# Performance work log

Hardware: AMD Instinct MI355X
Metric: run time of the kernel (lower is better)

Reference implementation:

```python
import jax, jax.numpy as jnp
import numpy as np

B, IC, H, W = 32, 128, 112, 112
OC, K, STRIDE, PAD = 256, 3, 2, 1


def setup_inputs() -> dict:
    key = jax.random.key(0)
    kx, kw = jax.random.split(key)
    x = jax.random.normal(kx, (B, IC, H, W), dtype=jnp.float32)
    weight = jax.random.normal(kw, (OC, IC, K, K), dtype=jnp.float32) * 0.01
    bias = jnp.zeros((OC,), dtype=jnp.float32)
    return {"x": x, "weight": weight, "bias": bias}


def reference(x, weight, bias):
    # Equivalent of the nested-loop conv: standard cross-correlation,
    # stride=2, zero padding=1, NCHW / OIHW layouts.
    out = jax.lax.conv_general_dilated(
        x, weight,
        window_strides=(STRIDE, STRIDE),
        padding=[(PAD, PAD), (PAD, PAD)],
        dimension_numbers=("NCHW", "OIHW", "NCHW"),
    )
    return out + bias[None, :, None, None]
```

## Files before the change

kernel.cpp:

```cpp
#include <hip/hip_runtime.h>
#include <hip/hip_bf16.h>


#define B_    32
#define IC_   128
#define H_    112
#define W_    112
#define HW_   (H_ * W_)
#define OC_   256
#define OH_   56
#define OW_   56
#define HP    113
#define NPIX  (B_ * OH_ * OW_)
#define XT_BYTES ((size_t)B_ * HP * HP * IC_ * 2)
#define WT_BYTES ((size_t)9 * OC_ * IC_ * 2)

typedef __attribute__((ext_vector_type(8))) short bf16x8;
typedef __attribute__((ext_vector_type(4))) float f32x4;

static __device__ __forceinline__ unsigned f2bf_u(float f) {
  union { float f; unsigned u; } v; v.f = f;
  return (v.u + 0x7FFF + ((v.u >> 16) & 1)) >> 16;
}

__global__ __launch_bounds__(256) void xtrans_kernel(
    const float* __restrict__ x, unsigned short* __restrict__ xt) {
  __shared__ unsigned short lds[128 * 128];
  const int ihp = blockIdx.x;
  const int b   = blockIdx.y;
  const int tid = threadIdx.x;

  if (ihp > 0) {
    const float* xp = x + (size_t)b * IC_ * HW_ + (size_t)(ihp - 1) * W_;
#pragma unroll
    for (int it = 0; it < 16; ++it) {
      const int i  = tid + it * 256;
      const int ic = i >> 5;
      const int g  = i & 31;
      if (g < 28) {
        const float4 v = *reinterpret_cast<const float4*>(
            xp + (size_t)ic * HW_ + g * 4);
        uint2 p;
        p.x = f2bf_u(v.x) | (f2bf_u(v.y) << 16);
        p.y = f2bf_u(v.z) | (f2bf_u(v.w) << 16);
        const int gs = g ^ (((ic >> 3) & 7) << 2);
        *reinterpret_cast<uint2*>(&lds[ic * 128 + gs * 4]) = p;
      }
    }
  }
  __syncthreads();

  unsigned short* xrow = xt + ((size_t)(b * HP + ihp)) * (HP * IC_);
  const bool live = (ihp > 0);
#pragma unroll
  for (int it = 0; it < 8; ++it) {
    const int e = tid + it * 256;
    if (e >= HP * 16) break;
    const int iwp = e >> 4;
    const int icg = e & 15;
    uint4 v = {0u, 0u, 0u, 0u};
    if (live && iwp > 0) {
      const int iw  = iwp - 1;
      const int col = ((iw >> 2) ^ ((icg & 7) << 2)) * 4 + (iw & 3);
      const int r0  = icg * 8;
      unsigned u0 = lds[(r0 + 0) * 128 + col];
      unsigned u1 = lds[(r0 + 1) * 128 + col];
      unsigned u2 = lds[(r0 + 2) * 128 + col];
      unsigned u3 = lds[(r0 + 3) * 128 + col];
      unsigned u4 = lds[(r0 + 4) * 128 + col];
      unsigned u5 = lds[(r0 + 5) * 128 + col];
      unsigned u6 = lds[(r0 + 6) * 128 + col];
      unsigned u7 = lds[(r0 + 7) * 128 + col];
      v.x = u0 | (u1 << 16);
      v.y = u2 | (u3 << 16);
      v.z = u4 | (u5 << 16);
      v.w = u6 | (u7 << 16);
    }
    *reinterpret_cast<uint4*>(xrow + iwp * IC_ + icg * 8) = v;
  }
}

__global__ __launch_bounds__(256) void wtrans_kernel(
    const float* __restrict__ w, unsigned short* __restrict__ wt) {
  const int t  = blockIdx.x * 256 + threadIdx.x;
  const int oc = t >> 7;
  const int ic = t & 127;
  const float* ws = w + (size_t)t * 9;
#pragma unroll
  for (int tap = 0; tap < 9; ++tap)
    wt[((size_t)tap * OC_ + oc) * IC_ + ic] = (unsigned short)f2bf_u(ws[tap]);
}

__global__ __launch_bounds__(256) void conv_mfma_kernel(
    const unsigned short* __restrict__ xt, const unsigned short* __restrict__ wt,
    const float* __restrict__ bias, float* __restrict__ out) {
  __shared__ short Ws[2][128 * 32];
  __shared__ short Xs[2][128 * 32];

  const int tid  = threadIdx.x;
  const int wav  = tid >> 6;
  const int lane = tid & 63;

  const int bid  = blockIdx.x;
  const int wgid = (bid & 7) * 196 + (bid >> 3);
  const int mt  = wgid & 1;
  const int pt  = wgid >> 1;
  const int oc0 = mt * 128;
  const int p0  = pt * 128;

  const int l2 = lane >> 2;
  const int lc = lane & 3;
  const char* xsrc[2];
  const char* wsrc[2];
#pragma unroll
  for (int i = 0; i < 2; ++i) {
    const int pix = p0 + wav * 32 + i * 16 + l2;
    const int b   = pix / 3136;
    const int q   = pix - b * 3136;
    const int oh  = q / 56;
    const int ow  = q - oh * 56;
    const size_t e = (((size_t)b * HP + 2 * oh) * HP + 2 * ow) * IC_;
    xsrc[i] = reinterpret_cast<const char*>(xt) + e * 2 + lc * 16;
    const int ocr = oc0 + wav * 32 + i * 16 + l2;
    wsrc[i] = reinterpret_cast<const char*>(wt) + (size_t)ocr * IC_ * 2 + lc * 16;
  }
  char* xdst = reinterpret_cast<char*>(&Xs[0][0]) + wav * 2048;
  char* wdst = reinterpret_cast<char*>(&Ws[0][0]) + wav * 2048;

  const int wm  = wav >> 1;
  const int wn  = wav & 1;
  const int l15 = lane & 15;
  const int kg  = (lane >> 4) * 8;
  const short* wrow = &Ws[0][0] + ((wm * 64 + l15) * 32 + kg);
  const short* xrow = &Xs[0][0] + ((wn * 64 + l15) * 32 + kg);

  f32x4 acc[4][4] = {};

  auto stage = [&](int buf, int tap, int icc) {
    const int kh = tap / 3;
    const int kw = tap - kh * 3;
    const size_t xoff = ((size_t)(kh * HP + kw) * IC_ + icc * 32) * 2;
    const size_t woff = ((size_t)tap * OC_ * IC_ + icc * 32) * 2;
    char* xd = xdst + buf * (128 * 32 * 2);
    char* wd = wdst + buf * (128 * 32 * 2);
#pragma unroll
    for (int i = 0; i < 2; ++i) {
      __builtin_amdgcn_global_load_lds(
          (const __attribute__((address_space(1))) void*)(xsrc[i] + xoff),
          (__attribute__((address_space(3))) void*)(xd + i * 1024), 16, 0, 0);
      __builtin_amdgcn_global_load_lds(
          (const __attribute__((address_space(1))) void*)(wsrc[i] + woff),
          (__attribute__((address_space(3))) void*)(wd + i * 1024), 16, 0, 0);
    }
  };

  auto compute = [&](int buf) {
    const short* wr = wrow + buf * (128 * 32);
    const short* xr = xrow + buf * (128 * 32);
    bf16x8 af[4], bfr[4];
#pragma unroll
    for (int mi = 0; mi < 4; ++mi)
      af[mi] = *reinterpret_cast<const bf16x8*>(wr + mi * 16 * 32);
#pragma unroll
    for (int ni = 0; ni < 4; ++ni)
      bfr[ni] = *reinterpret_cast<const bf16x8*>(xr + ni * 16 * 32);
#pragma unroll
    for (int mi = 0; mi < 4; ++mi)
#pragma unroll
      for (int ni = 0; ni < 4; ++ni)
        acc[mi][ni] = __builtin_amdgcn_mfma_f32_16x16x32_bf16(
            af[mi], bfr[ni], acc[mi][ni], 0, 0, 0);
  };

  stage(0, 0, 0);
  __syncthreads();

  for (int tap = 0; tap < 9; ++tap) {
    const bool lt = (tap == 8);
    stage(1, tap, 1);  compute(0);  __syncthreads();
    stage(0, tap, 2);  compute(1);  __syncthreads();
    stage(1, tap, 3);  compute(0);  __syncthreads();
    if (!lt) { stage(0, tap + 1, 0); }
    compute(1);
    if (!lt) { __syncthreads(); }
  }

#pragma unroll
  for (int mi = 0; mi < 4; ++mi) {
#pragma unroll
    for (int j = 0; j < 4; ++j) {
      const int oc = oc0 + wm * 64 + mi * 16 + (lane >> 4) * 4 + j;
      const float bv = bias[oc];
#pragma unroll
      for (int ni = 0; ni < 4; ++ni) {
        const int pix = p0 + wn * 64 + ni * 16 + l15;
        const int b   = pix / 3136;
        const int q   = pix - b * 3136;
        out[((size_t)b * OC_ + oc) * 3136 + q] = acc[mi][ni][j] + bv;
      }
    }
  }
}

__global__ __launch_bounds__(256) void conv2d_f32_kernel(
    const float* __restrict__ x, const float* __restrict__ w,
    const float* __restrict__ bias, float* __restrict__ out) {
  __shared__ float wlds[IC_ * 9][8];
  const int b   = blockIdx.z;
  const int oc0 = blockIdx.y * 8;
  const float* wsrc = w + (size_t)oc0 * (IC_ * 9);
  for (int i = threadIdx.x; i < IC_ * 9 * 8; i += 256) {
    const int j = i / (IC_ * 9);
    const int t = i - j * (IC_ * 9);
    wlds[t][j] = wsrc[(size_t)j * (IC_ * 9) + t];
  }
  __syncthreads();
  const int p  = blockIdx.x * 256 + threadIdx.x;
  const int ow = p % OW_;
  const int oh = p / OW_;
  const bool pv = (oh < OH_);
  const int ih0 = 2 * oh - 1;
  const int iw0 = 2 * ow - 1;
  const float* xb = x + (size_t)b * IC_ * HW_ + (ptrdiff_t)ih0 * W_ + iw0;
  float acc[8];
#pragma unroll
  for (int j = 0; j < 8; ++j) acc[j] = 0.f;
  for (int ic = 0; ic < IC_; ++ic) {
    const float* xc = xb + (size_t)ic * HW_;
#pragma unroll
    for (int kh = 0; kh < 3; ++kh) {
      const bool hv = pv && ((ih0 + kh) >= 0);
#pragma unroll
      for (int kw = 0; kw < 3; ++kw) {
        const bool v = hv && ((iw0 + kw) >= 0);
        const float xv = v ? xc[kh * W_ + kw] : 0.f;
        const int t = ic * 9 + kh * 3 + kw;
        const float4 w0 = *reinterpret_cast<const float4*>(&wlds[t][0]);
        const float4 w1 = *reinterpret_cast<const float4*>(&wlds[t][4]);
        acc[0] = fmaf(xv, w0.x, acc[0]); acc[1] = fmaf(xv, w0.y, acc[1]);
        acc[2] = fmaf(xv, w0.z, acc[2]); acc[3] = fmaf(xv, w0.w, acc[3]);
        acc[4] = fmaf(xv, w1.x, acc[4]); acc[5] = fmaf(xv, w1.y, acc[5]);
        acc[6] = fmaf(xv, w1.z, acc[6]); acc[7] = fmaf(xv, w1.w, acc[7]);
      }
    }
  }
  if (pv) {
#pragma unroll
    for (int j = 0; j < 8; ++j)
      out[(((size_t)(b * OC_ + oc0 + j)) * OH_ + oh) * OW_ + ow] =
          acc[j] + bias[oc0 + j];
  }
}

extern "C" void kernel_launch(void* const* d_in, const int* in_sizes, int n_in,
                              void* d_out, int out_size, void* d_ws, size_t ws_size,
                              hipStream_t stream) {
  const float* x    = (const float*)d_in[0];
  const float* w    = (const float*)d_in[1];
  const float* bias = (const float*)d_in[2];
  float* out        = (float*)d_out;

  if (ws_size >= XT_BYTES + WT_BYTES) {
    unsigned short* xt  = (unsigned short*)d_ws;
    unsigned short* wtp = (unsigned short*)((char*)d_ws + XT_BYTES);
    xtrans_kernel<<<dim3(HP, B_), 256, 0, stream>>>(x, xt);
    wtrans_kernel<<<128, 256, 0, stream>>>(w, wtp);
    conv_mfma_kernel<<<(NPIX / 128) * 2, 256, 0, stream>>>(xt, wtp, bias, out);
  } else {
    conv2d_f32_kernel<<<dim3(13, OC_ / 8, B_), 256, 0, stream>>>(x, w, bias, out);
  }
}
```

Before: 157.2 us.

## Deepen conv MFMA pipeline to 4 LDS stages with k-grouped weight layout

Weights are repacked into a k-group-major layout (step, 8-element k-chunk, oc) so both operand tiles share the same LDS layout, with one 16-byte chunk per lane per k-group. The main loop becomes a flat 36-step pipeline over four LDS buffers, staged two steps ahead. It replaces __syncthreads with explicit vmcnt waits plus one sched-fenced barrier per step, and adds launch_bounds occupancy of 2. This aims to hide global-load latency and cut barrier count, at the cost of doubled LDS use (64KB per block) and hand-tuned waitcnt correctness risk.

```diff
diff --git a/kernel.cpp b/kernel.cpp
--- a/kernel.cpp
+++ b/kernel.cpp
@@ -8,12 +8,10 @@
 #define W_    112
 #define HW_   (H_ * W_)
 #define OC_   256
-#define OH_   56
-#define OW_   56
 #define HP    113
-#define NPIX  (B_ * OH_ * OW_)
+#define NPIX  (B_ * 56 * 56)
 #define XT_BYTES ((size_t)B_ * HP * HP * IC_ * 2)
-#define WT_BYTES ((size_t)9 * OC_ * IC_ * 2)
+#define WT2_BYTES ((size_t)36 * 16384)
 
 typedef __attribute__((ext_vector_type(8))) short bf16x8;
 typedef __attribute__((ext_vector_type(4))) float f32x4;
@@ -80,26 +78,28 @@
   }
 }
 
-__global__ __launch_bounds__(256) void wtrans_kernel(
-    const float* __restrict__ w, unsigned short* __restrict__ wt) {
+__global__ __launch_bounds__(256) void wtrans2_kernel(
+    const float* __restrict__ w, unsigned short* __restrict__ wt2) {
   const int t  = blockIdx.x * 256 + threadIdx.x;
   const int oc = t >> 7;
   const int ic = t & 127;
+  const int icc = ic >> 5, q = (ic >> 3) & 3, e = ic & 7;
   const float* ws = w + (size_t)t * 9;
 #pragma unroll
-  for (int tap = 0; tap < 9; ++tap)
-    wt[((size_t)tap * OC_ + oc) * IC_ + ic] = (unsigned short)f2bf_u(ws[tap]);
-}
-
-__global__ __launch_bounds__(256) void conv_mfma_kernel(
-    const unsigned short* __restrict__ xt, const unsigned short* __restrict__ wt,
+  for (int tap = 0; tap < 9; ++tap) {
+    const int step = tap * 4 + icc;
+    wt2[((size_t)(step * 4 + q) * 256 + oc) * 8 + e] =
+        (unsigned short)f2bf_u(ws[tap]);
+  }
+}
+
+__global__ __launch_bounds__(256, 2) void conv_mfma_kernel(
+    const unsigned short* __restrict__ xt, const unsigned short* __restrict__ wt2,
     const float* __restrict__ bias, float* __restrict__ out) {
-  __shared__ short Ws[2][128 * 32];
-  __shared__ short Xs[2][128 * 32];
-
-  const int tid  = threadIdx.x;
-  const int wav  = tid >> 6;
-  const int lane = tid & 63;
+  __shared__ unsigned short Wl[4][4096];
+  __shared__ unsigned short Xl[4][4096];
+
+  const int tid = threadIdx.x, wav = tid >> 6, lane = tid & 63;
 
   const int bid  = blockIdx.x;
   const int wgid = (bid & 7) * 196 + (bid >> 3);
@@ -108,88 +108,92 @@
   const int oc0 = mt * 128;
   const int p0  = pt * 128;
 
-  const int l2 = lane >> 2;
-  const int lc = lane & 3;
   const char* xsrc[2];
-  const char* wsrc[2];
 #pragma unroll
   for (int i = 0; i < 2; ++i) {
-    const int pix = p0 + wav * 32 + i * 16 + l2;
+    const int pix = p0 + i * 64 + lane;
     const int b   = pix / 3136;
     const int q   = pix - b * 3136;
     const int oh  = q / 56;
     const int ow  = q - oh * 56;
     const size_t e = (((size_t)b * HP + 2 * oh) * HP + 2 * ow) * IC_;
-    xsrc[i] = reinterpret_cast<const char*>(xt) + e * 2 + lc * 16;
-    const int ocr = oc0 + wav * 32 + i * 16 + l2;
-    wsrc[i] = reinterpret_cast<const char*>(wt) + (size_t)ocr * IC_ * 2 + lc * 16;
-  }
-  char* xdst = reinterpret_cast<char*>(&Xs[0][0]) + wav * 2048;
-  char* wdst = reinterpret_cast<char*>(&Ws[0][0]) + wav * 2048;
-
-  const int wm  = wav >> 1;
-  const int wn  = wav & 1;
-  const int l15 = lane & 15;
-  const int kg  = (lane >> 4) * 8;
-  const short* wrow = &Ws[0][0] + ((wm * 64 + l15) * 32 + kg);
-  const short* xrow = &Xs[0][0] + ((wn * 64 + l15) * 32 + kg);
-
-  f32x4 acc[4][4] = {};
-
-  auto stage = [&](int buf, int tap, int icc) {
-    const int kh = tap / 3;
-    const int kw = tap - kh * 3;
+    xsrc[i] = reinterpret_cast<const char*>(xt) + e * 2 + wav * 16;
+  }
+  const char* wbase = reinterpret_cast<const char*>(wt2)
+                    + wav * 4096 + mt * 2048 + lane * 16;
+
+  auto stage = [&](int s, int buf) {
+    const int tap = s >> 2, icc = s & 3;
+    const int kh = tap / 3, kw = tap - kh * 3;
     const size_t xoff = ((size_t)(kh * HP + kw) * IC_ + icc * 32) * 2;
-    const size_t woff = ((size_t)tap * OC_ * IC_ + icc * 32) * 2;
-    char* xd = xdst + buf * (128 * 32 * 2);
-    char* wd = wdst + buf * (128 * 32 * 2);
+    const char* wsrc = wbase + (size_t)s * 16384;
+    char* xd = reinterpret_cast<char*>(&Xl[buf][0]) + wav * 2048;
+    char* wd = reinterpret_cast<char*>(&Wl[buf][0]) + wav * 2048;
 #pragma unroll
     for (int i = 0; i < 2; ++i) {
       __builtin_amdgcn_global_load_lds(
           (const __attribute__((address_space(1))) void*)(xsrc[i] + xoff),
           (__attribute__((address_space(3))) void*)(xd + i * 1024), 16, 0, 0);
       __builtin_amdgcn_global_load_lds(
-          (const __attribute__((address_space(1))) void*)(wsrc[i] + woff),
+          (const __attribute__((address_space(1))) void*)(wsrc + i * 1024),
           (__attribute__((address_space(3))) void*)(wd + i * 1024), 16, 0, 0);
     }
   };
 
+  const int wm = wav >> 1, wn = wav & 1;
+  const int l15 = lane & 15, lg = lane >> 4;
+
+  f32x4 acc[4][4] = {};
+
   auto compute = [&](int buf) {
-    const short* wr = wrow + buf * (128 * 32);
-    const short* xr = xrow + buf * (128 * 32);
-    bf16x8 af[4], bfr[4];
+    bf16x8 af[4], bx[4];
+    const unsigned short* wb  = &Wl[buf][0] + lg * 1024;
+    const unsigned short* xb2 = &Xl[buf][0] + lg * 1024;
 #pragma unroll
     for (int mi = 0; mi < 4; ++mi)
-      af[mi] = *reinterpret_cast<const bf16x8*>(wr + mi * 16 * 32);
+      af[mi] = *reinterpret_cast<const bf16x8*>(
+          wb + (wm * 64 + mi * 16 + l15) * 8);
 #pragma unroll
     for (int ni = 0; ni < 4; ++ni)
-      bfr[ni] = *reinterpret_cast<const bf16x8*>(xr + ni * 16 * 32);
+      bx[ni] = *reinterpret_cast<const bf16x8*>(
+          xb2 + (wn * 64 + ni * 16 + l15) * 8);
 #pragma unroll
     for (int mi = 0; mi < 4; ++mi)
 #pragma unroll
       for (int ni = 0; ni < 4; ++ni)
         acc[mi][ni] = __builtin_amdgcn_mfma_f32_16x16x32_bf16(
-            af[mi], bfr[ni], acc[mi][ni], 0, 0, 0);
+            af[mi], bx[ni], acc[mi][ni], 0, 0, 0);
   };
 
-  stage(0, 0, 0);
-  __syncthreads();
-
-  for (int tap = 0; tap < 9; ++tap) {
-    const bool lt = (tap == 8);
-    stage(1, tap, 1);  compute(0);  __syncthreads();
-    stage(0, tap, 2);  compute(1);  __syncthreads();
-    stage(1, tap, 3);  compute(0);  __syncthreads();
-    if (!lt) { stage(0, tap + 1, 0); }
-    compute(1);
-    if (!lt) { __syncthreads(); }
-  }
+#define FENCED_BARRIER()                          \
+  __builtin_amdgcn_sched_barrier(0);              \
+  __builtin_amdgcn_s_barrier();                   \
+  __builtin_amdgcn_sched_barrier(0)
+
+  stage(0, 0);
+  stage(1, 1);
+  asm volatile("s_waitcnt vmcnt(4)" ::: "memory");
+  FENCED_BARRIER();
+
+  for (int s = 0; s < 34; ++s) {
+    stage(s + 2, (s + 2) & 3);
+    asm volatile("s_waitcnt vmcnt(8)" ::: "memory");
+    FENCED_BARRIER();
+    compute(s & 3);
+  }
+  asm volatile("s_waitcnt vmcnt(4)" ::: "memory");
+  FENCED_BARRIER();
+  compute(34 & 3);
+  asm volatile("s_waitcnt vmcnt(0)" ::: "memory");
+  FENCED_BARRIER();
+  compute(35 & 3);
+#undef FENCED_BARRIER
 
 #pragma unroll
   for (int mi = 0; mi < 4; ++mi) {
 #pragma unroll
     for (int j = 0; j < 4; ++j) {
-      const int oc = oc0 + wm * 64 + mi * 16 + (lane >> 4) * 4 + j;
+      const int oc = oc0 + wm * 64 + mi * 16 + lg * 4 + j;
       const float bv = bias[oc];
 #pragma unroll
       for (int ni = 0; ni < 4; ++ni) {
@@ -216,9 +220,9 @@
   }
   __syncthreads();
   const int p  = blockIdx.x * 256 + threadIdx.x;
-  const int ow = p % OW_;
-  const int oh = p / OW_;
-  const bool pv = (oh < OH_);
+  const int ow = p % 56;
+  const int oh = p / 56;
+  const bool pv = (oh < 56);
   const int ih0 = 2 * oh - 1;
   const int iw0 = 2 * ow - 1;
   const float* xb = x + (size_t)b * IC_ * HW_ + (ptrdiff_t)ih0 * W_ + iw0;
@@ -247,7 +251,7 @@
   if (pv) {
 #pragma unroll
     for (int j = 0; j < 8; ++j)
-      out[(((size_t)(b * OC_ + oc0 + j)) * OH_ + oh) * OW_ + ow] =
+      out[(((size_t)(b * OC_ + oc0 + j)) * 56 + oh) * 56 + ow] =
           acc[j] + bias[oc0 + j];
   }
 }
@@ -260,12 +264,12 @@
   const float* bias = (const float*)d_in[2];
   float* out        = (float*)d_out;
 
-  if (ws_size >= XT_BYTES + WT_BYTES) {
+  if (ws_size >= XT_BYTES + WT2_BYTES) {
     unsigned short* xt  = (unsigned short*)d_ws;
-    unsigned short* wtp = (unsigned short*)((char*)d_ws + XT_BYTES);
+    unsigned short* wt2 = (unsigned short*)((char*)d_ws + XT_BYTES);
     xtrans_kernel<<<dim3(HP, B_), 256, 0, stream>>>(x, xt);
-    wtrans_kernel<<<128, 256, 0, stream>>>(w, wtp);
-    conv_mfma_kernel<<<(NPIX / 128) * 2, 256, 0, stream>>>(xt, wtp, bias, out);
+    wtrans2_kernel<<<128, 256, 0, stream>>>(w, wt2);
+    conv_mfma_kernel<<<NPIX / 64, 256, 0, stream>>>(xt, wt2, bias, out);
   } else {
     conv2d_f32_kernel<<<dim3(13, OC_ / 8, B_), 256, 0, stream>>>(x, w, bias, out);
   }
```

New measurement: 175.3 us. 11.5% more time.
